# Performance work log

Measured on AMD Instinct MI355X. Metric: run time of the kernel, lower is better.

Reference implementation:

```python
import jax, jax.numpy as jnp
import numpy as np

N, NB = 256, 8732  # batch, default boxes (SSD300)


def setup_inputs() -> dict:
    key = jax.random.key(0)
    k1, k2, k3, k4, k5 = jax.random.split(key, 5)
    ploc = jax.random.normal(k1, (N, 4, NB), dtype=jnp.float32)
    plabel = jax.random.normal(k2, (N, 1, NB), dtype=jnp.float32)
    # gloc / dboxes need strictly positive w,h (log / division); offset uniform
    gloc = jax.random.uniform(k3, (N, 4, NB), dtype=jnp.float32) + 0.1
    glabel = jax.random.randint(k4, (N, NB), 0, 2).astype(jnp.int64)
    dboxes = jax.random.uniform(k5, (1, 4, NB), dtype=jnp.float32) + 0.1
    return {"ploc": ploc, "plabel": plabel, "gloc": gloc,
            "glabel": glabel, "dboxes": dboxes}


def _bce_logits(x, y):
    # numerically stable BCEWithLogits, reduction='none'
    return jnp.maximum(x, 0.0) - x * y + jnp.log1p(jnp.exp(-jnp.abs(x)))


def _smooth_l1(d):
    ad = jnp.abs(d)
    return jnp.where(ad < 1.0, 0.5 * d * d, ad - 0.5)


def reference(ploc, plabel, gloc, glabel, dboxes):
    scale_xy = 1.0
    scale_wh = 1.0
    mask = glabel > 0                              # [N, NB] bool
    pos_num = mask.sum(axis=1)                     # [N] int

    # location target vector
    gxy = scale_xy * (gloc[:, :2, :] - dboxes[:, :2, :]) / dboxes[:, 2:, :]
    gwh = scale_wh * jnp.log(gloc[:, 2:, :] / dboxes[:, 2:, :])
    vec_gd = jnp.concatenate((gxy, gwh), axis=1)   # [N, 4, NB]

    sl1 = _smooth_l1(ploc - vec_gd).sum(axis=1)    # [N, NB]
    sl1 = (mask.astype(sl1.dtype) * sl1).sum(axis=1)  # [N]

    pl = plabel.squeeze(1).astype(jnp.float32)     # [N, NB]
    gl = glabel.astype(jnp.float32)
    con = _bce_logits(pl, gl)                      # [N, NB]

    # hard negative mining: rank negatives by loss, keep top 3*pos_num
    con_neg = jnp.where(mask, 0.0, con)
    con_idx = jnp.argsort(-con_neg, axis=1)        # descending sort indices
    con_rank = jnp.argsort(con_idx, axis=1)        # rank of each position
    neg_num = jnp.clip(3 * pos_num, None, NB)[:, None]
    neg_mask = con_rank < neg_num                  # [N, NB] bool

    keep = (mask | neg_mask).astype(con.dtype)
    closs = (con * keep).sum(axis=1)               # [N]

    total_loss = sl1 + closs
    num_mask = (pos_num > 0).astype(total_loss.dtype)
    pos_f = jnp.clip(pos_num.astype(total_loss.dtype), 1e-6, None)
    return (total_loss * num_mask / pos_f).mean(axis=0)
```

## Files before the change

### kernel.cpp

```cpp
#include <hip/hip_runtime.h>
#include <math.h>

#define N_ROWS 256
#define NB 8732
#define NB4 2183
#define CHUNKS 4
#define G_PER_CHUNK 546

__device__ __forceinline__ float smooth_l1(float d) {
    float ad = fabsf(d);
    return ad < 1.0f ? 0.5f * d * d : ad - 0.5f;
}

__device__ __forceinline__ float bce_y0(float x) {
    return fmaxf(x, 0.0f) + log1pf(expf(-fabsf(x)));
}

#define ELEMF(v, k) (((const float*)&(v))[k])
#define ELEMI(v, k) (((const int*)&(v))[k])

__global__ __launch_bounds__(256) void partial_kernel(
    const float* __restrict__ ploc, const float* __restrict__ plabel,
    const float* __restrict__ gloc, const int* __restrict__ glabel,
    const float* __restrict__ dboxes, float* __restrict__ ws) {
    const int row = blockIdx.x;
    const int chunk = blockIdx.y;
    const int tid = threadIdx.x;

    const int g0 = chunk * G_PER_CHUNK;
    const int g1 = min(g0 + G_PER_CHUNK, NB4);

    const float4* __restrict__ ploc4 = (const float4*)ploc;
    const float4* __restrict__ gloc4 = (const float4*)gloc;
    const float4* __restrict__ db4   = (const float4*)dboxes;
    const float4* __restrict__ pl4   = (const float4*)plabel;
    const int4*   __restrict__ gl4   = (const int4*)glabel;

    const int rb = row * 4 * NB4;
    const int rs = row * NB4;

    float sl1acc = 0.0f, conAll = 0.0f, conPos = 0.0f;
    int posCnt = 0;

    for (int g = g0 + tid; g < g1; g += 256) {
        float4 p0 = ploc4[rb + 0 * NB4 + g];
        float4 p1 = ploc4[rb + 1 * NB4 + g];
        float4 p2 = ploc4[rb + 2 * NB4 + g];
        float4 p3 = ploc4[rb + 3 * NB4 + g];
        float4 q0 = gloc4[rb + 0 * NB4 + g];
        float4 q1 = gloc4[rb + 1 * NB4 + g];
        float4 q2 = gloc4[rb + 2 * NB4 + g];
        float4 q3 = gloc4[rb + 3 * NB4 + g];
        float4 d0 = db4[0 * NB4 + g];
        float4 d1 = db4[1 * NB4 + g];
        float4 d2 = db4[2 * NB4 + g];
        float4 d3 = db4[3 * NB4 + g];
        int4   lb = gl4[rs + g];
        float4 px = pl4[rs + g];

#pragma unroll
        for (int k = 0; k < 4; ++k) {
            float w2 = ELEMF(d2, k);
            float w3 = ELEMF(d3, k);
            float gx = (ELEMF(q0, k) - ELEMF(d0, k)) / w2;
            float gy = (ELEMF(q1, k) - ELEMF(d1, k)) / w3;
            float gw = logf(ELEMF(q2, k) / w2);
            float gh = logf(ELEMF(q3, k) / w3);
            float s = smooth_l1(ELEMF(p0, k) - gx)
                    + smooth_l1(ELEMF(p1, k) - gy)
                    + smooth_l1(ELEMF(p2, k) - gw)
                    + smooth_l1(ELEMF(p3, k) - gh);
            int lab = ELEMI(lb, k);
            float x = ELEMF(px, k);
            float con = fmaxf(x, 0.0f) - x * (float)lab + log1pf(expf(-fabsf(x)));
            conAll += con;
            if (lab > 0) {
                posCnt += 1;
                sl1acc += s;
                conPos += con;
            }
        }
    }

    float v0 = sl1acc, v1 = conAll, v2 = conPos, v3 = (float)posCnt;
#pragma unroll
    for (int off = 32; off > 0; off >>= 1) {
        v0 += __shfl_down(v0, off);
        v1 += __shfl_down(v1, off);
        v2 += __shfl_down(v2, off);
        v3 += __shfl_down(v3, off);
    }
    __shared__ float sm[4][4];
    const int wid = tid >> 6, lane = tid & 63;
    if (lane == 0) {
        sm[wid][0] = v0; sm[wid][1] = v1; sm[wid][2] = v2; sm[wid][3] = v3;
    }
    __syncthreads();
    if (tid == 0) {
        float a0 = 0.f, a1 = 0.f, a2 = 0.f, a3 = 0.f;
#pragma unroll
        for (int w = 0; w < 4; ++w) {
            a0 += sm[w][0]; a1 += sm[w][1]; a2 += sm[w][2]; a3 += sm[w][3];
        }
        float* o = ws + (row * CHUNKS + chunk) * 4;
        o[0] = a0; o[1] = a1; o[2] = a2; o[3] = a3;
    }
}

__global__ __launch_bounds__(256) void final_kernel(
    const float* __restrict__ ws, const float* __restrict__ plabel,
    const int* __restrict__ glabel, float* __restrict__ out) {
    const int row = threadIdx.x;
    float sl1 = 0.f, conAll = 0.f, conPos = 0.f, posf = 0.f;
#pragma unroll
    for (int c = 0; c < CHUNKS; ++c) {
        const float* p = ws + (row * CHUNKS + c) * 4;
        sl1 += p[0]; conAll += p[1]; conPos += p[2]; posf += p[3];
    }
    const int pos = (int)(posf + 0.5f);
    const long long K = 3LL * (long long)pos;

    float closs;
    if (pos == 0) {
        closs = 0.0f;
    } else if (K >= (long long)NB) {
        closs = conAll;
    } else {
        const int Ki = (int)K;
        const float* plRow = plabel + row * NB;
        const int* glRow = glabel + row * NB;
        unsigned cur = 0;
        for (int bit = 31; bit >= 0; --bit) {
            unsigned trial = cur | (1u << bit);
            int cnt = 0;
            for (int j = 0; j < NB; ++j) {
                if (glRow[j] > 0) continue;
                float con = bce_y0(plRow[j]);
                if (__float_as_uint(con) >= trial) cnt++;
            }
            if (cnt >= Ki) cur = trial;
        }
        const float thr = __uint_as_float(cur);
        int cntG = 0; float sumG = 0.f;
        for (int j = 0; j < NB; ++j) {
            if (glRow[j] > 0) continue;
            float con = bce_y0(plRow[j]);
            if (con > thr) { cntG++; sumG += con; }
        }
        closs = conPos + sumG + (float)(Ki - cntG) * thr;
    }

    float loss = (pos > 0) ? (sl1 + closs) / (float)pos : 0.0f;

#pragma unroll
    for (int off = 32; off > 0; off >>= 1) loss += __shfl_down(loss, off);
    __shared__ float sm[4];
    const int wid = threadIdx.x >> 6, lane = threadIdx.x & 63;
    if (lane == 0) sm[wid] = loss;
    __syncthreads();
    if (threadIdx.x == 0) {
        float t = sm[0] + sm[1] + sm[2] + sm[3];
        out[0] = t * (1.0f / 256.0f);
    }
}

extern "C" void kernel_launch(void* const* d_in, const int* in_sizes, int n_in,
                              void* d_out, int out_size, void* d_ws, size_t ws_size,
                              hipStream_t stream) {
    const float* ploc   = (const float*)d_in[0];
    const float* plabel = (const float*)d_in[1];
    const float* gloc   = (const float*)d_in[2];
    const int*   glabel = (const int*)d_in[3];
    const float* dboxes = (const float*)d_in[4];
    float* ws  = (float*)d_ws;
    float* out = (float*)d_out;

    dim3 grid(N_ROWS, CHUNKS);
    hipLaunchKernelGGL(partial_kernel, grid, dim3(256), 0, stream,
                       ploc, plabel, gloc, glabel, dboxes, ws);
    hipLaunchKernelGGL(final_kernel, dim3(1), dim3(256), 0, stream,
                       ws, plabel, glabel, out);
}
```

Before: 27.07 us.

## Use fast math intrinsics, nontemporal loads, branchless masking and more chunks

Doubles the number of chunks per row so the partial kernel launches more blocks. Streaming inputs are read with nontemporal loads, while the small dboxes array stays on normal cached loads. Divisions and logs are replaced with hardware reciprocal and fast log/exp intrinsics, and the positive-label branch becomes multiply-by-mask. The fast intrinsics trade a little accuracy for fewer instructions, and the dominant cost is probably the single-block final_kernel radix select, which this leaves untouched.

```diff
diff --git a/kernel.cpp b/kernel.cpp
--- a/kernel.cpp
+++ b/kernel.cpp
@@ -4,8 +4,11 @@
 #define N_ROWS 256
 #define NB 8732
 #define NB4 2183
-#define CHUNKS 4
-#define G_PER_CHUNK 546
+#define CHUNKS 8
+#define G_PER_CHUNK 273
+
+typedef float f4 __attribute__((ext_vector_type(4)));
+typedef int   i4 __attribute__((ext_vector_type(4)));
 
 __device__ __forceinline__ float smooth_l1(float d) {
     float ad = fabsf(d);
@@ -15,9 +18,6 @@
 __device__ __forceinline__ float bce_y0(float x) {
     return fmaxf(x, 0.0f) + log1pf(expf(-fabsf(x)));
 }
-
-#define ELEMF(v, k) (((const float*)&(v))[k])
-#define ELEMI(v, k) (((const int*)&(v))[k])
 
 __global__ __launch_bounds__(256) void partial_kernel(
     const float* __restrict__ ploc, const float* __restrict__ plabel,
@@ -30,59 +30,59 @@
     const int g0 = chunk * G_PER_CHUNK;
     const int g1 = min(g0 + G_PER_CHUNK, NB4);
 
-    const float4* __restrict__ ploc4 = (const float4*)ploc;
-    const float4* __restrict__ gloc4 = (const float4*)gloc;
-    const float4* __restrict__ db4   = (const float4*)dboxes;
-    const float4* __restrict__ pl4   = (const float4*)plabel;
-    const int4*   __restrict__ gl4   = (const int4*)glabel;
+    const f4* __restrict__ ploc4 = (const f4*)ploc;
+    const f4* __restrict__ gloc4 = (const f4*)gloc;
+    const f4* __restrict__ db4   = (const f4*)dboxes;
+    const f4* __restrict__ pl4   = (const f4*)plabel;
+    const i4* __restrict__ gl4   = (const i4*)glabel;
 
     const int rb = row * 4 * NB4;
     const int rs = row * NB4;
 
     float sl1acc = 0.0f, conAll = 0.0f, conPos = 0.0f;
-    int posCnt = 0;
+    float posCnt = 0.0f;
 
     for (int g = g0 + tid; g < g1; g += 256) {
-        float4 p0 = ploc4[rb + 0 * NB4 + g];
-        float4 p1 = ploc4[rb + 1 * NB4 + g];
-        float4 p2 = ploc4[rb + 2 * NB4 + g];
-        float4 p3 = ploc4[rb + 3 * NB4 + g];
-        float4 q0 = gloc4[rb + 0 * NB4 + g];
-        float4 q1 = gloc4[rb + 1 * NB4 + g];
-        float4 q2 = gloc4[rb + 2 * NB4 + g];
-        float4 q3 = gloc4[rb + 3 * NB4 + g];
-        float4 d0 = db4[0 * NB4 + g];
-        float4 d1 = db4[1 * NB4 + g];
-        float4 d2 = db4[2 * NB4 + g];
-        float4 d3 = db4[3 * NB4 + g];
-        int4   lb = gl4[rs + g];
-        float4 px = pl4[rs + g];
+        f4 p0 = __builtin_nontemporal_load(&ploc4[rb + 0 * NB4 + g]);
+        f4 p1 = __builtin_nontemporal_load(&ploc4[rb + 1 * NB4 + g]);
+        f4 p2 = __builtin_nontemporal_load(&ploc4[rb + 2 * NB4 + g]);
+        f4 p3 = __builtin_nontemporal_load(&ploc4[rb + 3 * NB4 + g]);
+        f4 q0 = __builtin_nontemporal_load(&gloc4[rb + 0 * NB4 + g]);
+        f4 q1 = __builtin_nontemporal_load(&gloc4[rb + 1 * NB4 + g]);
+        f4 q2 = __builtin_nontemporal_load(&gloc4[rb + 2 * NB4 + g]);
+        f4 q3 = __builtin_nontemporal_load(&gloc4[rb + 3 * NB4 + g]);
+        f4 d0 = db4[0 * NB4 + g];
+        f4 d1 = db4[1 * NB4 + g];
+        f4 d2 = db4[2 * NB4 + g];
+        f4 d3 = db4[3 * NB4 + g];
+        i4 lb = __builtin_nontemporal_load(&gl4[rs + g]);
+        f4 px = __builtin_nontemporal_load(&pl4[rs + g]);
 
 #pragma unroll
         for (int k = 0; k < 4; ++k) {
-            float w2 = ELEMF(d2, k);
-            float w3 = ELEMF(d3, k);
-            float gx = (ELEMF(q0, k) - ELEMF(d0, k)) / w2;
-            float gy = (ELEMF(q1, k) - ELEMF(d1, k)) / w3;
-            float gw = logf(ELEMF(q2, k) / w2);
-            float gh = logf(ELEMF(q3, k) / w3);
-            float s = smooth_l1(ELEMF(p0, k) - gx)
-                    + smooth_l1(ELEMF(p1, k) - gy)
-                    + smooth_l1(ELEMF(p2, k) - gw)
-                    + smooth_l1(ELEMF(p3, k) - gh);
-            int lab = ELEMI(lb, k);
-            float x = ELEMF(px, k);
-            float con = fmaxf(x, 0.0f) - x * (float)lab + log1pf(expf(-fabsf(x)));
+            float rw2 = __builtin_amdgcn_rcpf(d2[k]);
+            float rw3 = __builtin_amdgcn_rcpf(d3[k]);
+            float gx = (q0[k] - d0[k]) * rw2;
+            float gy = (q1[k] - d1[k]) * rw3;
+            float gw = __logf(q2[k] * rw2);
+            float gh = __logf(q3[k] * rw3);
+            float s = smooth_l1(p0[k] - gx)
+                    + smooth_l1(p1[k] - gy)
+                    + smooth_l1(p2[k] - gw)
+                    + smooth_l1(p3[k] - gh);
+            int lab = lb[k];
+            float x = px[k];
+            float con = fmaxf(x, 0.0f) - x * (float)lab
+                      + __logf(1.0f + __expf(-fabsf(x)));
             conAll += con;
-            if (lab > 0) {
-                posCnt += 1;
-                sl1acc += s;
-                conPos += con;
-            }
+            float m = (lab > 0) ? 1.0f : 0.0f;
+            posCnt += m;
+            sl1acc += m * s;
+            conPos += m * con;
         }
     }
 
-    float v0 = sl1acc, v1 = conAll, v2 = conPos, v3 = (float)posCnt;
+    float v0 = sl1acc, v1 = conAll, v2 = conPos, v3 = posCnt;
 #pragma unroll
     for (int off = 32; off > 0; off >>= 1) {
         v0 += __shfl_down(v0, off);
```

Result: faster. 24.02 us (-11.3%).
